# Performance work log

Hardware: AMD Instinct MI355X
Metric: run time of the kernel (lower is better)

Reference implementation:

```python
import jax, jax.numpy as jnp
import numpy as np

N_NODES = 50000
N_EDGES = 500000
IN_CH = 128
HID = 64
HEADS = 4
N_LAYERS = 3
OUT_CH = 16
N_GRAPHS = 64
NEG_SLOPE = 0.2  # PyG GATConv default


def setup_inputs() -> dict:
    key = jax.random.key(0)
    ks = jax.random.split(key, 20)
    inp = {
        'x': jax.random.normal(ks[0], (N_NODES, IN_CH), dtype=jnp.float32),
        'edge_attr': jax.random.normal(ks[1], (N_EDGES, 8), dtype=jnp.float32),
        'edge_index': jax.random.randint(ks[2], (2, N_EDGES), 0, N_NODES, dtype=jnp.int64),
        'batch': jnp.sort(jax.random.randint(ks[3], (N_NODES,), 0, N_GRAPHS, dtype=jnp.int64)),
    }
    kidx = 4
    in_dim = IN_CH
    for i in range(N_LAYERS):
        inp[f'W{i}'] = jax.random.normal(ks[kidx], (in_dim, HEADS * HID), dtype=jnp.float32) * (1.0 / np.sqrt(in_dim)); kidx += 1
        inp[f'asrc{i}'] = jax.random.normal(ks[kidx], (HEADS, HID), dtype=jnp.float32) * 0.1; kidx += 1
        inp[f'adst{i}'] = jax.random.normal(ks[kidx], (HEADS, HID), dtype=jnp.float32) * 0.1; kidx += 1
        inp[f'b{i}'] = jnp.zeros((HEADS * HID,), dtype=jnp.float32)
        in_dim = HEADS * HID
    inp['Wc'] = jax.random.normal(ks[kidx], (HEADS * HID, OUT_CH), dtype=jnp.float32) * (1.0 / np.sqrt(HEADS * HID)); kidx += 1
    inp['bc'] = jnp.zeros((OUT_CH,), dtype=jnp.float32)
    return inp


def _gat_layer(x, src, dst, W, asrc, adst, b):
    # x: [N, F_in] -> h: [N, H, C]
    N = x.shape[0]
    h = (x @ W).reshape(N, HEADS, HID)
    s_src = jnp.einsum('nhc,hc->nh', h, asrc)  # [N, H]
    s_dst = jnp.einsum('nhc,hc->nh', h, adst)
    e = jax.nn.leaky_relu(s_src[src] + s_dst[dst], NEG_SLOPE)  # [E, H]
    # segment softmax over incoming edges of each destination node
    m = jax.ops.segment_max(e, dst, num_segments=N)            # [N, H]
    ex = jnp.exp(e - m[dst])
    denom = jax.ops.segment_sum(ex, dst, num_segments=N)       # [N, H]
    alpha = ex / (denom[dst] + 1e-16)                           # [E, H]
    out = jax.ops.segment_sum(alpha[:, :, None] * h[src], dst, num_segments=N)  # [N, H, C]
    return out.reshape(N, HEADS * HID) + b


def reference(x, edge_attr, edge_index, batch,
              W0, asrc0, adst0, b0,
              W1, asrc1, adst1, b1,
              W2, asrc2, adst2, b2,
              Wc, bc):
    N = x.shape[0]
    loop = jnp.arange(N, dtype=edge_index.dtype)
    # PyG GATConv adds self-loops by default
    src = jnp.concatenate([edge_index[0], loop])
    dst = jnp.concatenate([edge_index[1], loop])
    params = [(W0, asrc0, adst0, b0), (W1, asrc1, adst1, b1), (W2, asrc2, adst2, b2)]
    h = x
    for (W, asrc, adst, b) in params:
        h = jax.nn.relu(_gat_layer(h, src, dst, W, asrc, adst, b))
        # nn.Dropout(0.5) is identity in eval mode
    pooled = jax.ops.segment_sum(h, batch, num_segments=N_GRAPHS)  # global_add_pool
    return pooled @ Wc + bc
```

## Files before the change

### kernel.cpp

```cpp
#include <hip/hip_runtime.h>
#include <hip/hip_bf16.h>

#define NNODES 50000
#define NEDGES 500000
#define INCH 128
#define HID 64
#define HEADS 4
#define FDIM 256
#define NGRAPHS 64
#define OUTCH 16
#define NEG_SLOPE 0.2f

#define BM 64
#define BN 256
#define BK 32
#define APITCH 40

typedef float f32x4 __attribute__((ext_vector_type(4)));
typedef __bf16 bf16x8 __attribute__((ext_vector_type(8)));
typedef unsigned short u16x8 __attribute__((ext_vector_type(8)));

__device__ inline unsigned short f2bf_rne(float x) {
    unsigned int u = __float_as_uint(x);
    unsigned int r = (u + 0x7FFFu + ((u >> 16) & 1u)) >> 16;
    return (unsigned short)r;
}
__device__ inline float bf2f(unsigned short s) {
    return __uint_as_float(((unsigned int)s) << 16);
}
__device__ inline void split2(float x, unsigned short& h, unsigned short& l) {
    h = f2bf_rne(x);
    float hf = __uint_as_float(((unsigned int)h) << 16);
    l = f2bf_rne(x - hf);
}


__global__ void k_hist(const int* __restrict__ dst, int E, int* __restrict__ counts) {
    int i = blockIdx.x * blockDim.x + threadIdx.x;
    if (i < E) atomicAdd(&counts[dst[i]], 1);
}

__global__ __launch_bounds__(256) void k_blocksum(const int* __restrict__ counts, int N,
                                                  int* __restrict__ bsum) {
    int idx = blockIdx.x * 256 + threadIdx.x;
    int v = (idx < N) ? counts[idx] : 0;
#pragma unroll
    for (int off = 32; off; off >>= 1) v += __shfl_xor(v, off);
    __shared__ int wsum[4];
    if ((threadIdx.x & 63) == 0) wsum[threadIdx.x >> 6] = v;
    __syncthreads();
    if (threadIdx.x == 0) bsum[blockIdx.x] = wsum[0] + wsum[1] + wsum[2] + wsum[3];
}

__global__ __launch_bounds__(256) void k_scanfinal(const int* __restrict__ counts,
                                                   const int* __restrict__ bsum, int N,
                                                   int* __restrict__ rowstart) {
    __shared__ int tmp[256];
    __shared__ int wsum[4];
    int t = threadIdx.x, b = blockIdx.x;
    int p = 0;
    for (int i = t; i < b; i += 256) p += bsum[i];
#pragma unroll
    for (int off = 32; off; off >>= 1) p += __shfl_xor(p, off);
    int idx = b * 256 + t;
    int v = (idx < N) ? counts[idx] : 0;
    tmp[t] = v;
    if ((t & 63) == 0) wsum[t >> 6] = p;
    __syncthreads();
    int bp = wsum[0] + wsum[1] + wsum[2] + wsum[3];
    for (int off = 1; off < 256; off <<= 1) {
        int u = (t >= off) ? tmp[t - off] : 0;
        __syncthreads();
        tmp[t] += u;
        __syncthreads();
    }
    if (idx < N) rowstart[idx + 1] = bp + tmp[t];
    if (idx == 0) rowstart[0] = 0;
}

__global__ void k_scatter(const int* __restrict__ src, const int* __restrict__ dst, int E,
                          const int* __restrict__ rowstart, int* __restrict__ cursor,
                          int* __restrict__ csr_src) {
    int i = blockIdx.x * blockDim.x + threadIdx.x;
    if (i < E) {
        int d = dst[i];
        int p = atomicAdd(&cursor[d], 1);
        csr_src[rowstart[d] + p] = src[i];
    }
}


__global__ void k_wdecomp(const float* __restrict__ W, unsigned short* __restrict__ Wth,
                          unsigned short* __restrict__ Wtl, int K) {
    int i = blockIdx.x * 256 + threadIdx.x;
    if (i >= K * 256) return;
    int k = i >> 8, n = i & 255;
    unsigned short h, l;
    split2(W[i], h, l);
    Wth[n * K + k] = h;
    Wtl[n * K + k] = l;
}


__global__ __launch_bounds__(256) void k_gemm_mfma(
    const float* __restrict__ A, const unsigned short* __restrict__ Bh,
    const unsigned short* __restrict__ Bl, const float* __restrict__ av,
    const float* __restrict__ dv, unsigned short* __restrict__ Hb16,
    float* __restrict__ ssrcO, float* __restrict__ sdstO, int M, int K) {
    __shared__ unsigned short Ah[BM * APITCH];
    __shared__ unsigned short Al[BM * APITCH];
    __shared__ unsigned short Bhs[BN * APITCH];
    __shared__ unsigned short Bls[BN * APITCH];

    const int t = threadIdx.x;
    const int row0 = blockIdx.x * BM;
    const int wv = t >> 6, ln = t & 63, lr = ln & 15, lk = ln >> 4;

    const int arow = t >> 2, akb = t & 3;
    const int gr = min(row0 + arow, M - 1);

    f32x4 acc[4][4] = {};

    for (int k0 = 0; k0 < K; k0 += BK) {
        {
            const float* ap = A + (size_t)gr * K + k0 + akb * 8;
            float4 f0 = *(const float4*)(ap);
            float4 f1 = *(const float4*)(ap + 4);
            u16x8 hv, lv;
            float xs[8] = {f0.x, f0.y, f0.z, f0.w, f1.x, f1.y, f1.z, f1.w};
#pragma unroll
            for (int j = 0; j < 8; ++j) {
                unsigned short hh, ll;
                split2(xs[j], hh, ll);
                hv[j] = hh; lv[j] = ll;
            }
            *(u16x8*)&Ah[arow * APITCH + akb * 8] = hv;
            *(u16x8*)&Al[arow * APITCH + akb * 8] = lv;
        }
#pragma unroll
        for (int i = 0; i < 4; ++i) {
            int crow = (t >> 2) + i * 64;
            int kb = t & 3;
            *(u16x8*)&Bhs[crow * APITCH + kb * 8] =
                *(const u16x8*)(Bh + (size_t)crow * K + k0 + kb * 8);
            *(u16x8*)&Bls[crow * APITCH + kb * 8] =
                *(const u16x8*)(Bl + (size_t)crow * K + k0 + kb * 8);
        }
        __syncthreads();

        bf16x8 ah[4], al[4];
#pragma unroll
        for (int mi = 0; mi < 4; ++mi) {
            ah[mi] = *(const bf16x8*)&Ah[(mi * 16 + lr) * APITCH + lk * 8];
            al[mi] = *(const bf16x8*)&Al[(mi * 16 + lr) * APITCH + lk * 8];
        }
#pragma unroll
        for (int ni = 0; ni < 4; ++ni) {
            int brow = wv * 64 + ni * 16 + lr;
            bf16x8 bh = *(const bf16x8*)&Bhs[brow * APITCH + lk * 8];
            bf16x8 bl = *(const bf16x8*)&Bls[brow * APITCH + lk * 8];
#pragma unroll
            for (int mi = 0; mi < 4; ++mi) {
                acc[mi][ni] = __builtin_amdgcn_mfma_f32_16x16x32_bf16(ah[mi], bh, acc[mi][ni], 0, 0, 0);
                acc[mi][ni] = __builtin_amdgcn_mfma_f32_16x16x32_bf16(ah[mi], bl, acc[mi][ni], 0, 0, 0);
                acc[mi][ni] = __builtin_amdgcn_mfma_f32_16x16x32_bf16(al[mi], bh, acc[mi][ni], 0, 0, 0);
            }
        }
        __syncthreads();
    }

    float ps[4][4] = {}, pd[4][4] = {};
#pragma unroll
    for (int ni = 0; ni < 4; ++ni) {
        int col = wv * 64 + ni * 16 + lr;
        float a_s = av[col], a_d = dv[col];
#pragma unroll
        for (int mi = 0; mi < 4; ++mi) {
            f32x4 v = acc[mi][ni];
            int r = row0 + mi * 16 + lk * 4;
#pragma unroll
            for (int j = 0; j < 4; ++j) {
                if (r + j < M) Hb16[(size_t)(r + j) * FDIM + col] = f2bf_rne(v[j]);
                ps[mi][j] += v[j] * a_s;
                pd[mi][j] += v[j] * a_d;
            }
        }
    }
#pragma unroll
    for (int mi = 0; mi < 4; ++mi) {
#pragma unroll
        for (int j = 0; j < 4; ++j) {
            float s = ps[mi][j], q = pd[mi][j];
            s += __shfl_xor(s, 1); s += __shfl_xor(s, 2);
            s += __shfl_xor(s, 4); s += __shfl_xor(s, 8);
            q += __shfl_xor(q, 1); q += __shfl_xor(q, 2);
            q += __shfl_xor(q, 4); q += __shfl_xor(q, 8);
            if (lr == 0) {
                int r = row0 + mi * 16 + lk * 4 + j;
                if (r < M) {
                    ssrcO[r * HEADS + wv] = s;
                    sdstO[r * HEADS + wv] = q;
                }
            }
        }
    }
}


__global__ __launch_bounds__(256) void k_aggregate(const unsigned short* __restrict__ hb,
                                                   const float* __restrict__ ssrc,
                                                   const float* __restrict__ sdst,
                                                   const int* __restrict__ rowstart,
                                                   const int* __restrict__ csr_src,
                                                   const float* __restrict__ bias,
                                                   float* __restrict__ out, int N) {
    int wv = threadIdx.x >> 6, ln = threadIdx.x & 63;
    int n = blockIdx.x * 4 + wv;
    if (n >= N) return;
    int head = ln >> 4;
    int fo = head * 64 + (ln & 15) * 4;
    float sd = sdst[n * HEADS + head];
    float e = ssrc[n * HEADS + head] + sd;
    e = (e > 0.f) ? e : NEG_SLOPE * e;
    float m = e, d = 1.0f;
    ushort4 sv = *(const ushort4*)&hb[(size_t)n * FDIM + fo];
    float4 acc = make_float4(bf2f(sv.x), bf2f(sv.y), bf2f(sv.z), bf2f(sv.w));
    int r0 = rowstart[n], r1 = rowstart[n + 1];
    int r = r0;
    for (; r + 1 < r1; r += 2) {
        int s0 = csr_src[r], s1 = csr_src[r + 1];
        float sc0 = ssrc[s0 * HEADS + head] + sd;
        float sc1 = ssrc[s1 * HEADS + head] + sd;
        sc0 = (sc0 > 0.f) ? sc0 : NEG_SLOPE * sc0;
        sc1 = (sc1 > 0.f) ? sc1 : NEG_SLOPE * sc1;
        ushort4 u0 = *(const ushort4*)&hb[(size_t)s0 * FDIM + fo];
        ushort4 u1 = *(const ushort4*)&hb[(size_t)s1 * FDIM + fo];
        float mn = fmaxf(m, fmaxf(sc0, sc1));
        float wa = __expf(m - mn), w0 = __expf(sc0 - mn), w1 = __expf(sc1 - mn);
        acc.x = acc.x * wa + bf2f(u0.x) * w0 + bf2f(u1.x) * w1;
        acc.y = acc.y * wa + bf2f(u0.y) * w0 + bf2f(u1.y) * w1;
        acc.z = acc.z * wa + bf2f(u0.z) * w0 + bf2f(u1.z) * w1;
        acc.w = acc.w * wa + bf2f(u0.w) * w0 + bf2f(u1.w) * w1;
        d = d * wa + w0 + w1;
        m = mn;
    }
    if (r < r1) {
        int s0 = csr_src[r];
        float sc = ssrc[s0 * HEADS + head] + sd;
        sc = (sc > 0.f) ? sc : NEG_SLOPE * sc;
        ushort4 u0 = *(const ushort4*)&hb[(size_t)s0 * FDIM + fo];
        float mn = fmaxf(m, sc);
        float wa = __expf(m - mn), wn = __expf(sc - mn);
        acc.x = acc.x * wa + bf2f(u0.x) * wn;
        acc.y = acc.y * wa + bf2f(u0.y) * wn;
        acc.z = acc.z * wa + bf2f(u0.z) * wn;
        acc.w = acc.w * wa + bf2f(u0.w) * wn;
        d = d * wa + wn;
        m = mn;
    }
    float inv = 1.0f / d;
    float4 bv = *(const float4*)&bias[fo];
    float4 o;
    o.x = fmaxf(acc.x * inv + bv.x, 0.f);
    o.y = fmaxf(acc.y * inv + bv.y, 0.f);
    o.z = fmaxf(acc.z * inv + bv.z, 0.f);
    o.w = fmaxf(acc.w * inv + bv.w, 0.f);
    *(float4*)&out[(size_t)n * FDIM + fo] = o;
}


__global__ __launch_bounds__(256) void k_pool(const float* __restrict__ h,
                                              const int* __restrict__ batch,
                                              float* __restrict__ pooled, int N) {
    int f = threadIdx.x;
    int n0 = blockIdx.x * 128;
    if (n0 >= N) return;
    int n1 = min(n0 + 128, N);
    int g = batch[n0];
    float run = 0.f;
    for (int n = n0; n < n1; ++n) {
        int gn = batch[n];
        if (gn != g) {
            atomicAdd(&pooled[g * FDIM + f], run);
            run = 0.f;
            g = gn;
        }
        run += h[(size_t)n * FDIM + f];
    }
    atomicAdd(&pooled[g * FDIM + f], run);
}


__global__ __launch_bounds__(256) void k_final(const float* __restrict__ pooled,
                                               const float* __restrict__ Wc,
                                               const float* __restrict__ bc,
                                               float* __restrict__ out) {
    int tid = blockIdx.x * 256 + threadIdx.x;
    int g = tid >> 4, o = tid & 15;
    float s = bc[o];
    for (int k = 0; k < FDIM; ++k) s += pooled[g * FDIM + k] * Wc[k * OUTCH + o];
    out[g * OUTCH + o] = s;
}


extern "C" void kernel_launch(void* const* d_in, const int* in_sizes, int n_in,
                              void* d_out, int out_size, void* d_ws, size_t ws_size,
                              hipStream_t stream) {
    const float* x = (const float*)d_in[0];
    const int* edge_index = (const int*)d_in[2];
    const int* batch = (const int*)d_in[3];
    const float* W[3]    = {(const float*)d_in[4], (const float*)d_in[8],  (const float*)d_in[12]};
    const float* asrc[3] = {(const float*)d_in[5], (const float*)d_in[9],  (const float*)d_in[13]};
    const float* adst[3] = {(const float*)d_in[6], (const float*)d_in[10], (const float*)d_in[14]};
    const float* bias[3] = {(const float*)d_in[7], (const float*)d_in[11], (const float*)d_in[15]};
    const float* Wc = (const float*)d_in[16];
    const float* bc = (const float*)d_in[17];

    const int N = in_sizes[3];
    const int E = in_sizes[2] / 2;
    const int* e_src = edge_index;
    const int* e_dst = edge_index + E;

    char* ws = (char*)d_ws;
    size_t off = 0;
    unsigned short* hb = (unsigned short*)(ws + off); off += (size_t)N * FDIM * 2;
    float* outb = (float*)(ws + off); off += (size_t)N * FDIM * 4;
    float* ssrc = (float*)(ws + off); off += (size_t)N * HEADS * 4;
    float* sdst = (float*)(ws + off); off += (size_t)N * HEADS * 4;
    int* rowstart = (int*)(ws + off); off += ((size_t)(N + 1) * 4 + 255) / 256 * 256;
    int* cursor = (int*)(ws + off); off += (size_t)N * 4;
    int* csr_src = (int*)(ws + off); off += (size_t)E * 4;
    float* pooled = (float*)(ws + off); off += (size_t)NGRAPHS * FDIM * 4;
    int* bsum = (int*)(ws + off); off += ((size_t)((N + 255) / 256) * 4 + 255) / 256 * 256;
    unsigned short* Wth[3];
    unsigned short* Wtl[3];
    int Ks[3] = {INCH, FDIM, FDIM};
    for (int l = 0; l < 3; ++l) {
        Wth[l] = (unsigned short*)(ws + off); off += (size_t)256 * Ks[l] * 2;
        Wtl[l] = (unsigned short*)(ws + off); off += (size_t)256 * Ks[l] * 2;
    }

    const int nb = (N + 255) / 256;

    hipMemsetAsync(cursor, 0, (size_t)N * 4, stream);
    k_hist<<<(E + 255) / 256, 256, 0, stream>>>(e_dst, E, cursor);
    k_blocksum<<<nb, 256, 0, stream>>>(cursor, N, bsum);
    k_scanfinal<<<nb, 256, 0, stream>>>(cursor, bsum, N, rowstart);
    hipMemsetAsync(cursor, 0, (size_t)N * 4, stream);
    k_scatter<<<(E + 255) / 256, 256, 0, stream>>>(e_src, e_dst, E, rowstart, cursor, csr_src);

    for (int l = 0; l < 3; ++l)
        k_wdecomp<<<(Ks[l] * 256 + 255) / 256, 256, 0, stream>>>(W[l], Wth[l], Wtl[l], Ks[l]);

    const float* cur_in = x;
    for (int l = 0; l < 3; ++l) {
        int K = Ks[l];
        k_gemm_mfma<<<(N + BM - 1) / BM, 256, 0, stream>>>(cur_in, Wth[l], Wtl[l], asrc[l],
                                                           adst[l], hb, ssrc, sdst, N, K);
        k_aggregate<<<(N + 3) / 4, 256, 0, stream>>>(hb, ssrc, sdst, rowstart, csr_src,
                                                     bias[l], outb, N);
        cur_in = outb;
    }

    hipMemsetAsync(pooled, 0, (size_t)NGRAPHS * FDIM * 4, stream);
    k_pool<<<(N + 127) / 128, 256, 0, stream>>>(outb, batch, pooled, N);
    k_final<<<4, 256, 0, stream>>>(pooled, Wc, bc, (float*)d_out);
}
```

Before: 393.9 us.

## Pre-split activations to bf16 hi/lo and load GEMM tiles via direct-to-LDS

Activations are now split into bf16 hi/lo pairs once, in a separate pass for the input and in the aggregate epilogue for hidden layers, instead of inside every GEMM block. The GEMM then stages A and B tiles with global_load_lds 16-byte direct-to-LDS copies into an XOR-swizzled unpadded layout, which removes register round-trips and the in-loop conversion. The aggregate loop is also unrolled to four edges per iteration to expose more gather parallelism. This adds an extra pass over x and ping-pong hi/lo buffers, but the total bytes stored per layer stay the same as fp32.

```diff
diff --git a/kernel.cpp b/kernel.cpp
--- a/kernel.cpp
+++ b/kernel.cpp
@@ -14,11 +14,9 @@
 #define BM 64
 #define BN 256
 #define BK 32
-#define APITCH 40
 
 typedef float f32x4 __attribute__((ext_vector_type(4)));
 typedef __bf16 bf16x8 __attribute__((ext_vector_type(8)));
-typedef unsigned short u16x8 __attribute__((ext_vector_type(8)));
 
 __device__ inline unsigned short f2bf_rne(float x) {
     unsigned int u = __float_as_uint(x);
@@ -32,6 +30,10 @@
     h = f2bf_rne(x);
     float hf = __uint_as_float(((unsigned int)h) << 16);
     l = f2bf_rne(x - hf);
+}
+__device__ inline void gld_lds16(const void* g, void* l) {
+    __builtin_amdgcn_global_load_lds((__attribute__((address_space(1))) void*)g,
+                                     (__attribute__((address_space(3))) void*)l, 16, 0, 0);
 }
 
 
@@ -102,63 +104,68 @@
 }
 
 
+__global__ void k_adecomp(const float* __restrict__ X, unsigned short* __restrict__ Xh,
+                          unsigned short* __restrict__ Xl, int total4) {
+    int i = blockIdx.x * 256 + threadIdx.x;
+    if (i >= total4) return;
+    float4 v = ((const float4*)X)[i];
+    ushort4 h, l;
+    split2(v.x, h.x, l.x);
+    split2(v.y, h.y, l.y);
+    split2(v.z, h.z, l.z);
+    split2(v.w, h.w, l.w);
+    ((ushort4*)Xh)[i] = h;
+    ((ushort4*)Xl)[i] = l;
+}
+
+
 __global__ __launch_bounds__(256) void k_gemm_mfma(
-    const float* __restrict__ A, const unsigned short* __restrict__ Bh,
-    const unsigned short* __restrict__ Bl, const float* __restrict__ av,
-    const float* __restrict__ dv, unsigned short* __restrict__ Hb16,
+    const unsigned short* __restrict__ Aph, const unsigned short* __restrict__ Apl,
+    const unsigned short* __restrict__ Bph, const unsigned short* __restrict__ Bpl,
+    const float* __restrict__ av, const float* __restrict__ dv,
+    unsigned short* __restrict__ Hb16,
     float* __restrict__ ssrcO, float* __restrict__ sdstO, int M, int K) {
-    __shared__ unsigned short Ah[BM * APITCH];
-    __shared__ unsigned short Al[BM * APITCH];
-    __shared__ unsigned short Bhs[BN * APITCH];
-    __shared__ unsigned short Bls[BN * APITCH];
+    __shared__ unsigned short sAh[BM * BK];
+    __shared__ unsigned short sAl[BM * BK];
+    __shared__ unsigned short sBh[BN * BK];
+    __shared__ unsigned short sBl[BN * BK];
 
     const int t = threadIdx.x;
     const int row0 = blockIdx.x * BM;
     const int wv = t >> 6, ln = t & 63, lr = ln & 15, lk = ln >> 4;
 
-    const int arow = t >> 2, akb = t & 3;
-    const int gr = min(row0 + arow, M - 1);
+    const int ar = wv * 16 + (ln >> 2);
+    const int alc = (ln & 3) ^ ((ar >> 1) & 3);
+    const size_t agoff = (size_t)min(row0 + ar, M - 1) * K + alc * 8;
+    const int fsc = lk ^ ((lr >> 1) & 3);
 
     f32x4 acc[4][4] = {};
 
     for (int k0 = 0; k0 < K; k0 += BK) {
-        {
-            const float* ap = A + (size_t)gr * K + k0 + akb * 8;
-            float4 f0 = *(const float4*)(ap);
-            float4 f1 = *(const float4*)(ap + 4);
-            u16x8 hv, lv;
-            float xs[8] = {f0.x, f0.y, f0.z, f0.w, f1.x, f1.y, f1.z, f1.w};
-#pragma unroll
-            for (int j = 0; j < 8; ++j) {
-                unsigned short hh, ll;
-                split2(xs[j], hh, ll);
-                hv[j] = hh; lv[j] = ll;
-            }
-            *(u16x8*)&Ah[arow * APITCH + akb * 8] = hv;
-            *(u16x8*)&Al[arow * APITCH + akb * 8] = lv;
-        }
-#pragma unroll
-        for (int i = 0; i < 4; ++i) {
-            int crow = (t >> 2) + i * 64;
-            int kb = t & 3;
-            *(u16x8*)&Bhs[crow * APITCH + kb * 8] =
-                *(const u16x8*)(Bh + (size_t)crow * K + k0 + kb * 8);
-            *(u16x8*)&Bls[crow * APITCH + kb * 8] =
-                *(const u16x8*)(Bl + (size_t)crow * K + k0 + kb * 8);
+        gld_lds16(Aph + agoff + k0, &sAh[wv * 512]);
+        gld_lds16(Apl + agoff + k0, &sAl[wv * 512]);
+#pragma unroll
+        for (int j = 0; j < 4; ++j) {
+            int br = j * 64 + wv * 16 + (ln >> 2);
+            int blc = (ln & 3) ^ ((br >> 1) & 3);
+            size_t go = (size_t)br * K + k0 + blc * 8;
+            gld_lds16(Bph + go, &sBh[j * 2048 + wv * 512]);
+            gld_lds16(Bpl + go, &sBl[j * 2048 + wv * 512]);
         }
         __syncthreads();
 
         bf16x8 ah[4], al[4];
 #pragma unroll
         for (int mi = 0; mi < 4; ++mi) {
-            ah[mi] = *(const bf16x8*)&Ah[(mi * 16 + lr) * APITCH + lk * 8];
-            al[mi] = *(const bf16x8*)&Al[(mi * 16 + lr) * APITCH + lk * 8];
+            int r = mi * 16 + lr;
+            ah[mi] = *(const bf16x8*)&sAh[r * 32 + fsc * 8];
+            al[mi] = *(const bf16x8*)&sAl[r * 32 + fsc * 8];
         }
 #pragma unroll
         for (int ni = 0; ni < 4; ++ni) {
-            int brow = wv * 64 + ni * 16 + lr;
-            bf16x8 bh = *(const bf16x8*)&Bhs[brow * APITCH + lk * 8];
-            bf16x8 bl = *(const bf16x8*)&Bls[brow * APITCH + lk * 8];
+            int br = wv * 64 + ni * 16 + lr;
+            bf16x8 bh = *(const bf16x8*)&sBh[br * 32 + fsc * 8];
+            bf16x8 bl = *(const bf16x8*)&sBl[br * 32 + fsc * 8];
 #pragma unroll
             for (int mi = 0; mi < 4; ++mi) {
                 acc[mi][ni] = __builtin_amdgcn_mfma_f32_16x16x32_bf16(ah[mi], bh, acc[mi][ni], 0, 0, 0);
@@ -207,13 +214,12 @@
 }
 
 
-__global__ __launch_bounds__(256) void k_aggregate(const unsigned short* __restrict__ hb,
-                                                   const float* __restrict__ ssrc,
-                                                   const float* __restrict__ sdst,
-                                                   const int* __restrict__ rowstart,
-                                                   const int* __restrict__ csr_src,
-                                                   const float* __restrict__ bias,
-                                                   float* __restrict__ out, int N) {
+__global__ __launch_bounds__(256) void k_aggregate(
+    const unsigned short* __restrict__ hb,
+    const float* __restrict__ ssrc, const float* __restrict__ sdst,
+    const int* __restrict__ rowstart, const int* __restrict__ csr_src,
+    const float* __restrict__ bias,
+    unsigned short* __restrict__ oh, unsigned short* __restrict__ ol, int N) {
     int wv = threadIdx.x >> 6, ln = threadIdx.x & 63;
     int n = blockIdx.x * 4 + wv;
     if (n >= N) return;
@@ -227,24 +233,32 @@
     float4 acc = make_float4(bf2f(sv.x), bf2f(sv.y), bf2f(sv.z), bf2f(sv.w));
     int r0 = rowstart[n], r1 = rowstart[n + 1];
     int r = r0;
-    for (; r + 1 < r1; r += 2) {
-        int s0 = csr_src[r], s1 = csr_src[r + 1];
-        float sc0 = ssrc[s0 * HEADS + head] + sd;
-        float sc1 = ssrc[s1 * HEADS + head] + sd;
-        sc0 = (sc0 > 0.f) ? sc0 : NEG_SLOPE * sc0;
-        sc1 = (sc1 > 0.f) ? sc1 : NEG_SLOPE * sc1;
+    for (; r + 3 < r1; r += 4) {
+        int s0 = csr_src[r], s1 = csr_src[r + 1], s2 = csr_src[r + 2], s3 = csr_src[r + 3];
         ushort4 u0 = *(const ushort4*)&hb[(size_t)s0 * FDIM + fo];
         ushort4 u1 = *(const ushort4*)&hb[(size_t)s1 * FDIM + fo];
-        float mn = fmaxf(m, fmaxf(sc0, sc1));
-        float wa = __expf(m - mn), w0 = __expf(sc0 - mn), w1 = __expf(sc1 - mn);
-        acc.x = acc.x * wa + bf2f(u0.x) * w0 + bf2f(u1.x) * w1;
-        acc.y = acc.y * wa + bf2f(u0.y) * w0 + bf2f(u1.y) * w1;
-        acc.z = acc.z * wa + bf2f(u0.z) * w0 + bf2f(u1.z) * w1;
-        acc.w = acc.w * wa + bf2f(u0.w) * w0 + bf2f(u1.w) * w1;
-        d = d * wa + w0 + w1;
+        ushort4 u2 = *(const ushort4*)&hb[(size_t)s2 * FDIM + fo];
+        ushort4 u3 = *(const ushort4*)&hb[(size_t)s3 * FDIM + fo];
+        float c0 = ssrc[s0 * HEADS + head] + sd;
+        float c1 = ssrc[s1 * HEADS + head] + sd;
+        float c2 = ssrc[s2 * HEADS + head] + sd;
+        float c3 = ssrc[s3 * HEADS + head] + sd;
+        c0 = (c0 > 0.f) ? c0 : NEG_SLOPE * c0;
+        c1 = (c1 > 0.f) ? c1 : NEG_SLOPE * c1;
+        c2 = (c2 > 0.f) ? c2 : NEG_SLOPE * c2;
+        c3 = (c3 > 0.f) ? c3 : NEG_SLOPE * c3;
+        float mn = fmaxf(m, fmaxf(fmaxf(c0, c1), fmaxf(c2, c3)));
+        float wa = __expf(m - mn);
+        float w0 = __expf(c0 - mn), w1 = __expf(c1 - mn);
+        float w2 = __expf(c2 - mn), w3 = __expf(c3 - mn);
+        acc.x = acc.x * wa + bf2f(u0.x) * w0 + bf2f(u1.x) * w1 + bf2f(u2.x) * w2 + bf2f(u3.x) * w3;
+        acc.y = acc.y * wa + bf2f(u0.y) * w0 + bf2f(u1.y) * w1 + bf2f(u2.y) * w2 + bf2f(u3.y) * w3;
+        acc.z = acc.z * wa + bf2f(u0.z) * w0 + bf2f(u1.z) * w1 + bf2f(u2.z) * w2 + bf2f(u3.z) * w3;
+        acc.w = acc.w * wa + bf2f(u0.w) * w0 + bf2f(u1.w) * w1 + bf2f(u2.w) * w2 + bf2f(u3.w) * w3;
+        d = d * wa + ((w0 + w1) + (w2 + w3));
         m = mn;
     }
-    if (r < r1) {
+    for (; r < r1; ++r) {
         int s0 = csr_src[r];
         float sc = ssrc[s0 * HEADS + head] + sd;
         sc = (sc > 0.f) ? sc : NEG_SLOPE * sc;
@@ -260,16 +274,22 @@
     }
     float inv = 1.0f / d;
     float4 bv = *(const float4*)&bias[fo];
-    float4 o;
-    o.x = fmaxf(acc.x * inv + bv.x, 0.f);
-    o.y = fmaxf(acc.y * inv + bv.y, 0.f);
-    o.z = fmaxf(acc.z * inv + bv.z, 0.f);
-    o.w = fmaxf(acc.w * inv + bv.w, 0.f);
-    *(float4*)&out[(size_t)n * FDIM + fo] = o;
-}
-
-
-__global__ __launch_bounds__(256) void k_pool(const float* __restrict__ h,
+    float o0 = fmaxf(acc.x * inv + bv.x, 0.f);
+    float o1 = fmaxf(acc.y * inv + bv.y, 0.f);
+    float o2 = fmaxf(acc.z * inv + bv.z, 0.f);
+    float o3 = fmaxf(acc.w * inv + bv.w, 0.f);
+    ushort4 hh, ll;
+    split2(o0, hh.x, ll.x);
+    split2(o1, hh.y, ll.y);
+    split2(o2, hh.z, ll.z);
+    split2(o3, hh.w, ll.w);
+    *(ushort4*)&oh[(size_t)n * FDIM + fo] = hh;
+    *(ushort4*)&ol[(size_t)n * FDIM + fo] = ll;
+}
+
+
+__global__ __launch_bounds__(256) void k_pool(const unsigned short* __restrict__ oh,
+                                              const unsigned short* __restrict__ ol,
                                               const int* __restrict__ batch,
                                               float* __restrict__ pooled, int N) {
     int f = threadIdx.x;
@@ -285,7 +305,7 @@
             run = 0.f;
             g = gn;
         }
-        run += h[(size_t)n * FDIM + f];
+        run += bf2f(oh[(size_t)n * FDIM + f]) + bf2f(ol[(size_t)n * FDIM + f]);
     }
     atomicAdd(&pooled[g * FDIM + f], run);
 }
@@ -324,7 +344,12 @@
     char* ws = (char*)d_ws;
     size_t off = 0;
     unsigned short* hb = (unsigned short*)(ws + off); off += (size_t)N * FDIM * 2;
-    float* outb = (float*)(ws + off); off += (size_t)N * FDIM * 4;
+    unsigned short* xh = (unsigned short*)(ws + off); off += (size_t)N * INCH * 2;
+    unsigned short* xl = (unsigned short*)(ws + off); off += (size_t)N * INCH * 2;
+    unsigned short* P0h = (unsigned short*)(ws + off); off += (size_t)N * FDIM * 2;
+    unsigned short* P0l = (unsigned short*)(ws + off); off += (size_t)N * FDIM * 2;
+    unsigned short* P1h = (unsigned short*)(ws + off); off += (size_t)N * FDIM * 2;
+    unsigned short* P1l = (unsigned short*)(ws + off); off += (size_t)N * FDIM * 2;
     float* ssrc = (float*)(ws + off); off += (size_t)N * HEADS * 4;
     float* sdst = (float*)(ws + off); off += (size_t)N * HEADS * 4;
     int* rowstart = (int*)(ws + off); off += ((size_t)(N + 1) * 4 + 255) / 256 * 256;
@@ -349,20 +374,25 @@
     hipMemsetAsync(cursor, 0, (size_t)N * 4, stream);
     k_scatter<<<(E + 255) / 256, 256, 0, stream>>>(e_src, e_dst, E, rowstart, cursor, csr_src);
 
+    k_adecomp<<<((N * INCH / 4) + 255) / 256, 256, 0, stream>>>(x, xh, xl, N * INCH / 4);
     for (int l = 0; l < 3; ++l)
         k_wdecomp<<<(Ks[l] * 256 + 255) / 256, 256, 0, stream>>>(W[l], Wth[l], Wtl[l], Ks[l]);
 
-    const float* cur_in = x;
+    const unsigned short* Ah = xh;
+    const unsigned short* Al = xl;
+    unsigned short* Oh[3] = {P0h, P1h, P0h};
+    unsigned short* Ol[3] = {P0l, P1l, P0l};
     for (int l = 0; l < 3; ++l) {
         int K = Ks[l];
-        k_gemm_mfma<<<(N + BM - 1) / BM, 256, 0, stream>>>(cur_in, Wth[l], Wtl[l], asrc[l],
+        k_gemm_mfma<<<(N + BM - 1) / BM, 256, 0, stream>>>(Ah, Al, Wth[l], Wtl[l], asrc[l],
                                                            adst[l], hb, ssrc, sdst, N, K);
         k_aggregate<<<(N + 3) / 4, 256, 0, stream>>>(hb, ssrc, sdst, rowstart, csr_src,
-                                                     bias[l], outb, N);
-        cur_in = outb;
+                                                     bias[l], Oh[l], Ol[l], N);
+        Ah = Oh[l];
+        Al = Ol[l];
     }
 
     hipMemsetAsync(pooled, 0, (size_t)NGRAPHS * FDIM * 4, stream);
-    k_pool<<<(N + 127) / 128, 256, 0, stream>>>(outb, batch, pooled, N);
+    k_pool<<<(N + 127) / 128, 256, 0, stream>>>(P0h, P0l, batch, pooled, N);
     k_final<<<4, 256, 0, stream>>>(pooled, Wc, bc, (float*)d_out);
 }
```

Result: no change. 393.7 us (-0.0%).
